# Kernel optimization log

Hardware: AMD Instinct MI355X
Metric: run time of the kernel (lower is better)

## Reference

```python
import jax, jax.numpy as jnp
import numpy as np

B, S, D, H = 2, 2048, 1024, 16
HD = D // H  # head_dim = 64


def setup_inputs() -> dict:
    key = jax.random.key(0)
    ks = jax.random.split(key, 10)
    s = 1.0 / np.sqrt(D)
    # causal mask: 0 on/below diagonal, -inf above (matches masked_fill(mask == -inf))
    neg_inf = jnp.float32(-jnp.inf)
    mask = jnp.where(jnp.tril(jnp.ones((S, S), dtype=bool)), 0.0, neg_inf).astype(jnp.float32)
    return {
        "x": jax.random.normal(ks[0], (B, S, D), dtype=jnp.float32),
        "mask": mask,
        "Wq": jax.random.uniform(ks[1], (D, D), jnp.float32, -s, s),
        "bq": jax.random.uniform(ks[2], (D,), jnp.float32, -s, s),
        "Wk": jax.random.uniform(ks[3], (D, D), jnp.float32, -s, s),
        "bk": jax.random.uniform(ks[4], (D,), jnp.float32, -s, s),
        "Wv": jax.random.uniform(ks[5], (D, D), jnp.float32, -s, s),
        "bv": jax.random.uniform(ks[6], (D,), jnp.float32, -s, s),
        "Wo": jax.random.uniform(ks[7], (D, D), jnp.float32, -s, s),
        "bo": jax.random.uniform(ks[8], (D,), jnp.float32, -s, s),
    }


def reference(x, mask, Wq, bq, Wk, bk, Wv, bv, Wo, bo):
    b, s, d = x.shape
    scale = jnp.float32(HD) ** 0.5
    # qkv projections (torch Linear: y = x W^T + b), split into heads: [b, H, s, hd]
    q = (x @ Wq.T + bq).reshape(b, s, H, HD).transpose(0, 2, 1, 3)
    k = (x @ Wk.T + bk).reshape(b, s, H, HD).transpose(0, 2, 1, 3)
    v = (x @ Wv.T + bv).reshape(b, s, H, HD).transpose(0, 2, 1, 3)
    scores = jnp.einsum("bhqd,bhkd->bhqk", q, k) / scale
    scores = jnp.where(mask[None, None] == -jnp.inf, -jnp.inf, scores)
    attn = jax.nn.softmax(scores, axis=-1)
    # dropout(p=0.1) is identity in eval mode
    ctx = jnp.einsum("bhqk,bhkd->bhqd", attn, v)
    ctx = ctx.transpose(0, 2, 1, 3).reshape(b, s, d)
    return ctx @ Wo.T + bo
```

## Files before the change

kernel.cpp:

```cpp
#include <hip/hip_runtime.h>
#include <hip/hip_bf16.h>
#include <cmath>

#define S_ 2048
#define D_ 1024
#define H_ 16
#define HD_ 64
#define GM 4096
#define GN 1024
#define GK 1024
#define QSCALE 0.1803368801111f
#define THR2   11.5415603f

typedef __attribute__((ext_vector_type(4))) float f32x4;
typedef __attribute__((ext_vector_type(8))) short bf16x8;
typedef __attribute__((ext_vector_type(4))) short bf16x4;

__device__ __forceinline__ short f2bf(float f) {
    union { float f; unsigned u; } x; x.f = f;
    unsigned r = x.u + 0x7fffu + ((x.u >> 16) & 1u);
    return (short)(r >> 16);
}
__device__ __forceinline__ short bftrunc(float f) {
    union { float f; unsigned u; } x; x.f = f;
    return (short)(x.u >> 16);
}
__device__ __forceinline__ void gload16(const short* g, short* l) {
    __builtin_amdgcn_global_load_lds((const __attribute__((address_space(1))) void*)g,
                                     (__attribute__((address_space(3))) void*)l, 16, 0, 0);
}

__global__ __launch_bounds__(256) void cvt_all(
    const float* __restrict__ x,
    const float* __restrict__ w0, const float* __restrict__ w1,
    const float* __restrict__ w2, const float* __restrict__ w3,
    short* __restrict__ xb, short* __restrict__ Wb)
{
    const int bid = blockIdx.x;
    const float* src; short* dst; int loc;
    if (bid < 2048) { src = x; dst = xb; loc = bid; }
    else {
        int wsel = (bid - 2048) >> 9, wb = (bid - 2048) & 511;
        src = wsel == 0 ? w0 : wsel == 1 ? w1 : wsel == 2 ? w2 : w3;
        dst = Wb + ((size_t)wsel << 20);
        loc = wb;
    }
    int id = loc * 256 + threadIdx.x;
    const float* s = src + (size_t)id * 8;
    f32x4 a = *(const f32x4*)s;
    f32x4 b = *(const f32x4*)(s + 4);
    bf16x8 h;
    h[0] = f2bf(a[0]); h[1] = f2bf(a[1]); h[2] = f2bf(a[2]); h[3] = f2bf(a[3]);
    h[4] = f2bf(b[0]); h[5] = f2bf(b[1]); h[6] = f2bf(b[2]); h[7] = f2bf(b[3]);
    *(bf16x8*)(dst + (size_t)id * 8) = h;
}

__global__ __launch_bounds__(256) void gemm_qkv(
    const short* __restrict__ A, const short* __restrict__ W3,
    const float* __restrict__ bq, const float* __restrict__ bk, const float* __restrict__ bv,
    short* __restrict__ Qb, short* __restrict__ Kb, short* __restrict__ Vt)
{
    __shared__ short SMEM[17408];
    short* As = SMEM;
    short* Bs = SMEM + 8192;
    const int t = threadIdx.x, lane = t & 63, w = t >> 6;
    const int bid = blockIdx.x;
    const int xcd = bid & 7, idx = bid >> 3;
    const int ntile = idx % 24, mloc = idx / 24;
    const int m0 = (xcd * 4 + mloc) * 128;
    const int n0g = ntile * 128;
    const int wr = (w >> 1) * 64, wc = (w & 1) * 64;
    const int fr = lane & 15, g = lane >> 4;
    const int srow = lane >> 3;
    const int gslot = (lane & 7) ^ srow;
    const int rbase = w * 32;

    f32x4 acc[4][4] = {};

    for (int kt = 0; kt < GK; kt += 64) {
        __syncthreads();
        #pragma unroll
        for (int i = 0; i < 4; ++i) {
            int row = rbase + i * 8 + srow;
            gload16(A  + (size_t)(m0 + row) * GK + kt + gslot * 8, &As[(rbase + i * 8) * 64]);
            gload16(W3 + (size_t)(n0g + row) * GK + kt + gslot * 8, &Bs[(rbase + i * 8) * 64]);
        }
        __syncthreads();
        #pragma unroll
        for (int ks = 0; ks < 2; ++ks) {
            bf16x8 af[4], bf_[4];
            #pragma unroll
            for (int mb = 0; mb < 4; ++mb) {
                int row = wr + mb * 16 + fr;
                af[mb] = *(const bf16x8*)((const char*)As + row * 128 + (((ks * 4 + g) ^ (row & 7)) << 4));
            }
            #pragma unroll
            for (int nb = 0; nb < 4; ++nb) {
                int row = wc + nb * 16 + fr;
                bf_[nb] = *(const bf16x8*)((const char*)Bs + row * 128 + (((ks * 4 + g) ^ (row & 7)) << 4));
            }
            #pragma unroll
            for (int mb = 0; mb < 4; ++mb)
                #pragma unroll
                for (int nb = 0; nb < 4; ++nb)
                    acc[mb][nb] = __builtin_amdgcn_mfma_f32_16x16x32_bf16(
                        af[mb], bf_[nb], acc[mb][nb], 0, 0, 0);
        }
    }

    const int seg = n0g >> 10, nn = n0g & 1023;
    if (seg == 2) {
        __syncthreads();
        short* Cs = SMEM;
        #pragma unroll
        for (int mb = 0; mb < 4; ++mb)
            #pragma unroll
            for (int nb = 0; nb < 4; ++nb) {
                int cl = wc + nb * 16 + fr;
                int rl_ = wr + mb * 16 + g * 4;
                float bvv = bv[nn + cl];
                bf16x4 hv;
                #pragma unroll
                for (int r = 0; r < 4; ++r) hv[r] = f2bf(acc[mb][nb][r] + bvv);
                *(bf16x4*)(Cs + cl * 136 + rl_) = hv;
            }
        __syncthreads();
        const int b = m0 >> 11;
        const int s_base = m0 & 2047;
        #pragma unroll
        for (int p = 0; p < 8; ++p) {
            int id = t + p * 256;
            int cl = id >> 4, ch = id & 15;
            int n = nn + cl;
            int h = n >> 6, d = n & 63;
            bf16x8 v = *(const bf16x8*)(Cs + cl * 136 + ch * 8);
            *(bf16x8*)(Vt + ((size_t)((b * 16 + h) * 64 + d)) * S_ + s_base + ch * 8) = v;
        }
    } else {
        const float* bp = seg ? bk : bq;
        short* dst = seg ? Kb : Qb;
        const float sc = seg ? 1.0f : QSCALE;
        #pragma unroll
        for (int mb = 0; mb < 4; ++mb)
            #pragma unroll
            for (int nb = 0; nb < 4; ++nb) {
                int grow = m0 + wr + mb * 16 + g * 4;
                int gcol = nn + wc + nb * 16 + fr;
                float bvv = bp[gcol];
                #pragma unroll
                for (int r = 0; r < 4; ++r)
                    dst[(size_t)(grow + r) * GN + gcol] = f2bf((acc[mb][nb][r] + bvv) * sc);
            }
    }
}

__global__ __launch_bounds__(256) void gemm_o(
    const short* __restrict__ A, const short* __restrict__ W,
    const float* __restrict__ bias, float* __restrict__ C)
{
    __shared__ short As[2][8192];
    __shared__ short Bs[2][8192];
    const int t = threadIdx.x, lane = t & 63, w = t >> 6;
    const int bid = blockIdx.x;
    const int xcd = bid & 7, wk = bid >> 3;
    const int m0 = (xcd * 4 + (wk & 3)) * 128;
    const int n0 = (wk >> 2) * 128;
    const int wr = (w >> 1) * 64, wc = (w & 1) * 64;
    const int fr = lane & 15, g = lane >> 4;
    const int srow = lane >> 3;
    const int gslot = (lane & 7) ^ srow;
    const int rbase = w * 32;

    f32x4 acc[4][4] = {};

    #pragma unroll
    for (int i = 0; i < 4; ++i) {
        int row = rbase + i * 8 + srow;
        gload16(A + (size_t)(m0 + row) * GK + gslot * 8, &As[0][(rbase + i * 8) * 64]);
        gload16(W + (size_t)(n0 + row) * GK + gslot * 8, &Bs[0][(rbase + i * 8) * 64]);
    }
    __syncthreads();

    int cur = 0;
    for (int t64 = 0; t64 < 16; ++t64) {
        if (t64 < 15) {
            int kt = (t64 + 1) * 64;
            #pragma unroll
            for (int i = 0; i < 4; ++i) {
                int row = rbase + i * 8 + srow;
                gload16(A + (size_t)(m0 + row) * GK + kt + gslot * 8, &As[cur ^ 1][(rbase + i * 8) * 64]);
                gload16(W + (size_t)(n0 + row) * GK + kt + gslot * 8, &Bs[cur ^ 1][(rbase + i * 8) * 64]);
            }
        }
        #pragma unroll
        for (int ks = 0; ks < 2; ++ks) {
            bf16x8 af[4], bf_[4];
            #pragma unroll
            for (int mb = 0; mb < 4; ++mb) {
                int row = wr + mb * 16 + fr;
                af[mb] = *(const bf16x8*)((const char*)&As[cur][0] + row * 128 + (((ks * 4 + g) ^ (row & 7)) << 4));
            }
            #pragma unroll
            for (int nb = 0; nb < 4; ++nb) {
                int row = wc + nb * 16 + fr;
                bf_[nb] = *(const bf16x8*)((const char*)&Bs[cur][0] + row * 128 + (((ks * 4 + g) ^ (row & 7)) << 4));
            }
            #pragma unroll
            for (int mb = 0; mb < 4; ++mb)
                #pragma unroll
                for (int nb = 0; nb < 4; ++nb)
                    acc[mb][nb] = __builtin_amdgcn_mfma_f32_16x16x32_bf16(
                        af[mb], bf_[nb], acc[mb][nb], 0, 0, 0);
        }
        __syncthreads();
        cur ^= 1;
    }

    #pragma unroll
    for (int mb = 0; mb < 4; ++mb)
        #pragma unroll
        for (int nb = 0; nb < 4; ++nb) {
            int grow = m0 + wr + mb * 16 + g * 4;
            int gcol = n0 + wc + nb * 16 + fr;
            float bvv = bias[gcol];
            #pragma unroll
            for (int r = 0; r < 4; ++r)
                C[(size_t)(grow + r) * GN + gcol] = acc[mb][nb][r] + bvv;
        }
}

__global__ __launch_bounds__(256) void attn_fwd_bf16(
    const short* __restrict__ Qb, const short* __restrict__ Kb,
    const short* __restrict__ Vtb, short* __restrict__ Ob)
{
    __shared__ short SK[2][4096];
    __shared__ short SVT[2][4096];
    __shared__ short SP[4][1024];

    const int t = threadIdx.x, lane = t & 63, w = t >> 6;
    const int g = lane >> 4, fr = lane & 15;
    const int bid = blockIdx.x;
    const int xcd = bid & 7, idx = bid >> 3;
    const int bh = xcd * 4 + (idx & 3);
    const int qt = 31 - (idx >> 2);
    const int b = bh >> 4, h = bh & 15;
    const int q0 = qt * 64;
    const int wq0 = w * 16;
    const int nt = qt + 1;

    bf16x8 qf[2];
    #pragma unroll
    for (int ks = 0; ks < 2; ++ks)
        qf[ks] = *(const bf16x8*)(Qb + (size_t)(b * S_ + q0 + wq0 + fr) * D_
                                  + h * 64 + ks * 32 + g * 8);

    const int srow8 = lane >> 3;
    const short* kp[2];
    const short* vp[2];
    short* kd0[2]; short* kd1[2]; short* vd0[2]; short* vd1[2];
    #pragma unroll
    for (int i = 0; i < 2; ++i) {
        int row = w * 16 + i * 8 + srow8;
        int gsl = (lane & 7) ^ (row & 7);
        kp[i] = Kb + (size_t)(b * S_ + row) * D_ + h * 64 + gsl * 8;
        vp[i] = Vtb + (size_t)(bh * 64 + row) * S_ + gsl * 8;
        kd0[i] = &SK[0][(w * 16 + i * 8) * 64];  kd1[i] = &SK[1][(w * 16 + i * 8) * 64];
        vd0[i] = &SVT[0][(w * 16 + i * 8) * 64]; vd1[i] = &SVT[1][(w * 16 + i * 8) * 64];
    }
    short* SPw = &SP[w][0];
    const int qsw = fr & 7;

    #pragma unroll
    for (int i = 0; i < 2; ++i) {
        gload16(kp[i], kd0[i]);
        gload16(vp[i], vd0[i]);
    }
    __syncthreads();

    f32x4 Oacc[4] = {};
    float m2 = -1e30f, lsum = 0.f;
    int cur = 0;

    for (int kt = 0; kt < nt; ++kt) {
        if (kt + 1 < nt) {
            kp[0] += 64 * D_; kp[1] += 64 * D_;
            vp[0] += 64;      vp[1] += 64;
            if (cur) {
                #pragma unroll
                for (int i = 0; i < 2; ++i) { gload16(kp[i], kd0[i]); gload16(vp[i], vd0[i]); }
            } else {
                #pragma unroll
                for (int i = 0; i < 2; ++i) { gload16(kp[i], kd1[i]); gload16(vp[i], vd1[i]); }
            }
        }
        const char* SKc = (const char*)(cur ? &SK[1][0] : &SK[0][0]);
        const char* SVc = (const char*)(cur ? &SVT[1][0] : &SVT[0][0]);

        f32x4 sacc[4] = {};
        #pragma unroll
        for (int ks = 0; ks < 2; ++ks) {
            #pragma unroll
            for (int mk = 0; mk < 4; ++mk) {
                int row = mk * 16 + fr;
                bf16x8 kf = *(const bf16x8*)(SKc + row * 128 + (((ks * 4 + g) ^ (row & 7)) << 4));
                sacc[mk] = __builtin_amdgcn_mfma_f32_16x16x32_bf16(kf, qf[ks], sacc[mk], 0, 0, 0);
            }
        }
        if (kt == qt) {
            #pragma unroll
            for (int mk = 0; mk < 4; ++mk)
                #pragma unroll
                for (int r = 0; r < 4; ++r)
                    if (mk * 16 + g * 4 + r > wq0 + fr) sacc[mk][r] = -1e30f;
        }

        float rm = -1e30f;
        #pragma unroll
        for (int mk = 0; mk < 4; ++mk)
            #pragma unroll
            for (int r = 0; r < 4; ++r) rm = fmaxf(rm, sacc[mk][r]);
        rm = fmaxf(rm, __shfl_xor(rm, 16));
        rm = fmaxf(rm, __shfl_xor(rm, 32));
        if (rm > m2 + THR2) {
            float resc = exp2f(m2 - rm);
            m2 = rm;
            lsum *= resc;
            #pragma unroll
            for (int md = 0; md < 4; ++md)
                #pragma unroll
                for (int r = 0; r < 4; ++r) Oacc[md][r] *= resc;
        }
        float ps = 0.f;
        #pragma unroll
        for (int mk = 0; mk < 4; ++mk) {
            bf16x4 pk;
            #pragma unroll
            for (int r = 0; r < 4; ++r) {
                float pe = exp2f(sacc[mk][r] - m2);
                ps += pe;
                pk[r] = bftrunc(pe);
            }
            int k = mk * 16 + g * 4;
            *(bf16x4*)((char*)SPw + fr * 128 + (((k >> 3) ^ qsw) << 4) + ((k & 7) << 1)) = pk;
        }
        ps += __shfl_xor(ps, 16);
        ps += __shfl_xor(ps, 32);
        lsum += ps;

        #pragma unroll
        for (int ks = 0; ks < 2; ++ks) {
            bf16x8 pf = *(const bf16x8*)((const char*)SPw + fr * 128 + (((ks * 4 + g) ^ qsw) << 4));
            #pragma unroll
            for (int md = 0; md < 4; ++md) {
                int row = md * 16 + fr;
                bf16x8 vf = *(const bf16x8*)(SVc + row * 128 + (((ks * 4 + g) ^ (row & 7)) << 4));
                Oacc[md] = __builtin_amdgcn_mfma_f32_16x16x32_bf16(vf, pf, Oacc[md], 0, 0, 0);
            }
        }
        __syncthreads();
        cur ^= 1;
    }

    const float rl = 1.f / lsum;
    const size_t orow = (size_t)(b * S_ + q0 + wq0 + fr) * D_ + h * 64;
    #pragma unroll
    for (int md = 0; md < 4; ++md) {
        bf16x4 ov;
        #pragma unroll
        for (int r = 0; r < 4; ++r) ov[r] = f2bf(Oacc[md][r] * rl);
        *(bf16x4*)(Ob + orow + md * 16 + g * 4) = ov;
    }
}

extern "C" void kernel_launch(void* const* d_in, const int* in_sizes, int n_in,
                              void* d_out, int out_size, void* d_ws, size_t ws_size,
                              hipStream_t stream)
{
    const float* x  = (const float*)d_in[0];
    const float* Wq = (const float*)d_in[2];
    const float* bq = (const float*)d_in[3];
    const float* Wk = (const float*)d_in[4];
    const float* bk = (const float*)d_in[5];
    const float* Wv = (const float*)d_in[6];
    const float* bv = (const float*)d_in[7];
    const float* Wo = (const float*)d_in[8];
    const float* bo = (const float*)d_in[9];
    float* out = (float*)d_out;

    const size_t MD = (size_t)GM * D_;
    short* xb = (short*)d_ws;
    short* Wb = xb + MD;
    short* Qb = Wb + 4 * (size_t)D_ * D_;
    short* Kb = Qb + MD;
    short* Vt = Kb + MD;
    short* Ob = Vt + MD;

    dim3 blk(256);
    cvt_all<<<dim3(4096), blk, 0, stream>>>(x, Wq, Wk, Wv, Wo, xb, Wb);
    gemm_qkv<<<dim3(768), blk, 0, stream>>>(xb, Wb, bq, bk, bv, Qb, Kb, Vt);
    attn_fwd_bf16<<<dim3(1024), blk, 0, stream>>>(Qb, Kb, Vt, Ob);
    gemm_o<<<dim3(256), blk, 0, stream>>>(Ob, Wb + 3 * (size_t)D_ * D_, bo, out);
}
```

Before: 122.3 us.

## Load K and V fragments directly from global memory into registers in attention

```diff
diff --git a/kernel.cpp b/kernel.cpp
--- a/kernel.cpp
+++ b/kernel.cpp
@@ -233,8 +233,6 @@
     const short* __restrict__ Qb, const short* __restrict__ Kb,
     const short* __restrict__ Vtb, short* __restrict__ Ob)
 {
-    __shared__ short SK[2][4096];
-    __shared__ short SVT[2][4096];
     __shared__ short SP[4][1024];
 
     const int t = threadIdx.x, lane = t & 63, w = t >> 6;
@@ -254,58 +252,39 @@
         qf[ks] = *(const bf16x8*)(Qb + (size_t)(b * S_ + q0 + wq0 + fr) * D_
                                   + h * 64 + ks * 32 + g * 8);
 
-    const int srow8 = lane >> 3;
-    const short* kp[2];
-    const short* vp[2];
-    short* kd0[2]; short* kd1[2]; short* vd0[2]; short* vd1[2];
-    #pragma unroll
-    for (int i = 0; i < 2; ++i) {
-        int row = w * 16 + i * 8 + srow8;
-        int gsl = (lane & 7) ^ (row & 7);
-        kp[i] = Kb + (size_t)(b * S_ + row) * D_ + h * 64 + gsl * 8;
-        vp[i] = Vtb + (size_t)(bh * 64 + row) * S_ + gsl * 8;
-        kd0[i] = &SK[0][(w * 16 + i * 8) * 64];  kd1[i] = &SK[1][(w * 16 + i * 8) * 64];
-        vd0[i] = &SVT[0][(w * 16 + i * 8) * 64]; vd1[i] = &SVT[1][(w * 16 + i * 8) * 64];
-    }
+    const short* kb = Kb + (size_t)(b * S_ + fr) * D_ + h * 64 + g * 8;
+    const short* vb = Vtb + (size_t)(bh * 64 + fr) * S_ + g * 8;
+
     short* SPw = &SP[w][0];
     const int qsw = fr & 7;
 
-    #pragma unroll
-    for (int i = 0; i < 2; ++i) {
-        gload16(kp[i], kd0[i]);
-        gload16(vp[i], vd0[i]);
-    }
-    __syncthreads();
-
     f32x4 Oacc[4] = {};
     float m2 = -1e30f, lsum = 0.f;
-    int cur = 0;
 
     for (int kt = 0; kt < nt; ++kt) {
-        if (kt + 1 < nt) {
-            kp[0] += 64 * D_; kp[1] += 64 * D_;
-            vp[0] += 64;      vp[1] += 64;
-            if (cur) {
-                #pragma unroll
-                for (int i = 0; i < 2; ++i) { gload16(kp[i], kd0[i]); gload16(vp[i], vd0[i]); }
-            } else {
-                #pragma unroll
-                for (int i = 0; i < 2; ++i) { gload16(kp[i], kd1[i]); gload16(vp[i], vd1[i]); }
-            }
-        }
-        const char* SKc = (const char*)(cur ? &SK[1][0] : &SK[0][0]);
-        const char* SVc = (const char*)(cur ? &SVT[1][0] : &SVT[0][0]);
+        bf16x8 kf[2][4];
+        #pragma unroll
+        for (int ks = 0; ks < 2; ++ks)
+            #pragma unroll
+            for (int mk = 0; mk < 4; ++mk)
+                kf[ks][mk] = *(const bf16x8*)(kb + mk * 16 * D_ + ks * 32);
+        kb += 64 * D_;
 
         f32x4 sacc[4] = {};
         #pragma unroll
-        for (int ks = 0; ks < 2; ++ks) {
-            #pragma unroll
-            for (int mk = 0; mk < 4; ++mk) {
-                int row = mk * 16 + fr;
-                bf16x8 kf = *(const bf16x8*)(SKc + row * 128 + (((ks * 4 + g) ^ (row & 7)) << 4));
-                sacc[mk] = __builtin_amdgcn_mfma_f32_16x16x32_bf16(kf, qf[ks], sacc[mk], 0, 0, 0);
-            }
-        }
+        for (int ks = 0; ks < 2; ++ks)
+            #pragma unroll
+            for (int mk = 0; mk < 4; ++mk)
+                sacc[mk] = __builtin_amdgcn_mfma_f32_16x16x32_bf16(kf[ks][mk], qf[ks], sacc[mk], 0, 0, 0);
+
+        bf16x8 vf[2][4];
+        #pragma unroll
+        for (int ks = 0; ks < 2; ++ks)
+            #pragma unroll
+            for (int md = 0; md < 4; ++md)
+                vf[ks][md] = *(const bf16x8*)(vb + md * 16 * S_ + ks * 32);
+        vb += 64;
+
         if (kt == qt) {
             #pragma unroll
             for (int mk = 0; mk < 4; ++mk)
@@ -351,14 +330,9 @@
         for (int ks = 0; ks < 2; ++ks) {
             bf16x8 pf = *(const bf16x8*)((const char*)SPw + fr * 128 + (((ks * 4 + g) ^ qsw) << 4));
             #pragma unroll
-            for (int md = 0; md < 4; ++md) {
-                int row = md * 16 + fr;
-                bf16x8 vf = *(const bf16x8*)(SVc + row * 128 + (((ks * 4 + g) ^ (row & 7)) << 4));
-                Oacc[md] = __builtin_amdgcn_mfma_f32_16x16x32_bf16(vf, pf, Oacc[md], 0, 0, 0);
-            }
-        }
-        __syncthreads();
-        cur ^= 1;
+            for (int md = 0; md < 4; ++md)
+                Oacc[md] = __builtin_amdgcn_mfma_f32_16x16x32_bf16(vf[ks][md], pf, Oacc[md], 0, 0, 0);
+        }
     }
 
     const float rl = 1.f / lsum;
```

Result: slower. 220.2 us (+80.0%).
